# Kernel optimization log

Hardware: AMD Instinct MI355X
Metric: run time of the kernel (lower is better)

The kernel has to match this reference:

```python
import jax, jax.numpy as jnp
import numpy as np

N = 50000
E = 800000
IN_C, HID, LAT = 256, 128, 64


def setup_inputs() -> dict:
    key = jax.random.key(0)
    ks = jax.random.split(key, 8)
    x = jax.random.normal(ks[0], (N, IN_C), dtype=jnp.float32)
    edge_index = jax.random.randint(ks[1], (2, E), 0, N, dtype=jnp.int64)
    # Glorot-ish scaled weights (PyG GCNConv: Linear weight + separate bias)
    W1 = jax.random.normal(ks[2], (IN_C, HID), dtype=jnp.float32) / np.sqrt(IN_C)
    b1 = jnp.zeros((HID,), dtype=jnp.float32)
    Wmu = jax.random.normal(ks[3], (HID, LAT), dtype=jnp.float32) / np.sqrt(HID)
    bmu = jnp.zeros((LAT,), dtype=jnp.float32)
    Wlv = jax.random.normal(ks[4], (HID, LAT), dtype=jnp.float32) / np.sqrt(HID)
    blv = jnp.zeros((LAT,), dtype=jnp.float32)
    return {"x": x, "edge_index": edge_index, "W1": W1, "b1": b1,
            "Wmu": Wmu, "bmu": bmu, "Wlv": Wlv, "blv": blv}


def gcn_conv(x, edge_index, W, b):
    """PyG GCNConv: add self-loops, sym-normalize, transform, scatter-add."""
    n = x.shape[0]
    loop = jnp.arange(n, dtype=edge_index.dtype)
    row = jnp.concatenate([edge_index[0], loop])  # source
    col = jnp.concatenate([edge_index[1], loop])  # target
    deg = jax.ops.segment_sum(jnp.ones_like(col, dtype=x.dtype), col, num_segments=n)
    dinv = jax.lax.rsqrt(jnp.maximum(deg, 1e-12))  # deg >= 1 due to self-loops
    norm = dinv[row] * dinv[col]                   # [E+N]
    h = x @ W                                      # transform first (smaller width)
    msg = h[row] * norm[:, None]                   # [E+N, out] gathered messages
    out = jax.ops.segment_sum(msg, col, num_segments=n)
    return out + b


def reference(x, edge_index, W1, b1, Wmu, bmu, Wlv, blv):
    h = jax.nn.relu(gcn_conv(x, edge_index, W1, b1))
    # dropout p=0.0 -> identity
    mu = gcn_conv(h, edge_index, Wmu, bmu)
    logvar = gcn_conv(h, edge_index, Wlv, blv)
    return (mu, logvar)
```

## Files before the change

### kernel.cpp

```cpp
#include <hip/hip_runtime.h>
#include <stdint.h>

#define NN   50000
#define NE   800000
#define INC  256
#define HID  128
#define LAT  64

typedef unsigned short u16;
typedef short v8s __attribute__((ext_vector_type(8)));
typedef float v4f __attribute__((ext_vector_type(4)));

#define SLAB_OFF 0
#define OFFS_OFF 802816
#define W1P_OFF  881216
#define W2P_OFF  897600
#define G1_OFF   905792

#define NBIN        196
#define OFFS_STRIDE 200
#define NSLAB       784

#define G2_OFFU  8388608
#define C2_CNT   8388608
#define C2_DINV  8438608
#define C2_BKT   8488608

#define GB    782

__device__ __forceinline__ u16 f2b(float f) {
    union { float f; uint32_t i; } c; c.f = f;
    uint32_t r = c.i + 0x7FFF + ((c.i >> 16) & 1);
    return (u16)(r >> 16);
}
__device__ __forceinline__ float blo(unsigned u) { return __uint_as_float(u << 16); }
__device__ __forceinline__ float bhi(unsigned u) { return __uint_as_float(u & 0xffff0000u); }

__device__ void pack1_body(const float* __restrict__ W1, u16* __restrict__ W1P, int b) {
    int tg = b * 256 + threadIdx.x;
    int ks = tg >> 9, rem = tg & 511;
    int nt = rem >> 6, lane = rem & 63;
    int quad = lane >> 4, l15 = lane & 15;
    u16 o[8];
    #pragma unroll
    for (int j = 0; j < 8; j++)
        o[j] = f2b(W1[(long)(ks * 32 + quad * 8 + j) * HID + nt * 16 + l15]);
    *(ushort4*)(W1P + (long)tg * 8)     = make_ushort4(o[0], o[1], o[2], o[3]);
    *(ushort4*)(W1P + (long)tg * 8 + 4) = make_ushort4(o[4], o[5], o[6], o[7]);
}

__device__ void pack2_body(const float* __restrict__ Wmu, const float* __restrict__ Wlv,
                           u16* __restrict__ W2P, int b) {
    int tg = b * 256 + threadIdx.x;
    int ks = tg >> 9, rem = tg & 511;
    int nt = rem >> 6, lane = rem & 63;
    int quad = lane >> 4, l15 = lane & 15;
    const float* W = (nt < 4) ? Wmu : Wlv;
    int ntl = (nt < 4) ? nt : nt - 4;
    u16 o[8];
    #pragma unroll
    for (int j = 0; j < 8; j++)
        o[j] = f2b(W[(long)(ks * 32 + quad * 8 + j) * LAT + ntl * 16 + l15]);
    *(ushort4*)(W2P + (long)tg * 8)     = make_ushort4(o[0], o[1], o[2], o[3]);
    *(ushort4*)(W2P + (long)tg * 8 + 4) = make_ushort4(o[4], o[5], o[6], o[7]);
}

__global__ __launch_bounds__(256) void k_fusedA(unsigned* csr, const float* W1,
        const float* Wmu, const float* Wlv) {
    int b = blockIdx.x;
    if (b < 16) pack1_body(W1, (u16*)(csr + W1P_OFF), b);
    else pack2_body(Wmu, Wlv, (u16*)(csr + W2P_OFF), b - 16);
}

__device__ void gemm1_body(const float* __restrict__ xbuf,
        const unsigned* __restrict__ csr, u16* __restrict__ g1, int blk,
        u16* __restrict__ As) {
    const u16* W1P = (const u16*)(csr + W1P_OFF);
    int tid = threadIdx.x;
    int m0b = blk * 64;
    #pragma unroll
    for (int i = 0; i < 16; i++) {
        int idx = i * 256 + tid;
        int r = idx >> 6, c4 = idx & 63;
        int gr = m0b + r; gr = gr < NN ? gr : NN - 1;
        float4 a = *(const float4*)(xbuf + (long)gr * INC + c4 * 4);
        *(ushort4*)(As + r * 264 + c4 * 4) =
            make_ushort4(f2b(a.x), f2b(a.y), f2b(a.z), f2b(a.w));
    }
    __syncthreads();
    int lane = tid & 63, w = tid >> 6;
    int quad = lane >> 4, l15 = lane & 15;
    int m0 = m0b + w * 16;
    const v8s* bp = (const v8s*)W1P;
    v4f acc[8];
    #pragma unroll
    for (int t = 0; t < 8; t++) acc[t] = (v4f){0.f, 0.f, 0.f, 0.f};
    #pragma unroll
    for (int ks = 0; ks < 8; ks++) {
        v8s af = *(const v8s*)(As + (w * 16 + l15) * 264 + ks * 32 + quad * 8);
        #pragma unroll
        for (int t = 0; t < 8; t++) {
            v8s bf = bp[(ks * 8 + t) * 64 + lane];
            acc[t] = __builtin_amdgcn_mfma_f32_16x16x32_bf16(af, bf, acc[t], 0, 0, 0);
        }
    }
    #pragma unroll
    for (int r = 0; r < 4; r++) {
        int rr = m0 + quad * 4 + r;
        if (rr < NN) {
            u16* dst = g1 + (long)rr * HID + l15;
            #pragma unroll
            for (int t = 0; t < 8; t++) dst[t * 16] = f2b(acc[t][r]);
        }
    }
}

__device__ void part_body(const int* __restrict__ row, const int* __restrict__ col,
                          unsigned* __restrict__ csr, int id,
                          int* hist, int* scanbuf, unsigned* recs) {
    int tid = threadIdx.x;
    int base = id * 1024;
    hist[tid] = 0;
    __syncthreads();
    int v[4], u[4];
    #pragma unroll
    for (int i = 0; i < 4; i++) {
        int e = base + i * 256 + tid;
        if (e < NE) {
            v[i] = col[e]; u[i] = row[e];
            atomicAdd(&hist[v[i] >> 8], 1);
        } else v[i] = -1;
    }
    __syncthreads();
    int x = hist[tid];
    scanbuf[tid] = x;
    __syncthreads();
    for (int s = 1; s < 256; s <<= 1) {
        int y = (tid >= s) ? scanbuf[tid - s] : 0;
        __syncthreads();
        scanbuf[tid] += y;
        __syncthreads();
    }
    int excl = scanbuf[tid] - x;
    u16* offs = (u16*)(csr + OFFS_OFF) + (long)id * OFFS_STRIDE;
    if (tid <= NBIN) offs[tid] = (u16)excl;
    hist[tid] = excl;
    __syncthreads();
    #pragma unroll
    for (int i = 0; i < 4; i++) {
        if (v[i] >= 0) {
            int slot = atomicAdd(&hist[v[i] >> 8], 1);
            recs[slot] = (unsigned)u[i] | ((unsigned)(v[i] & 255) << 16);
        }
    }
    __syncthreads();
    unsigned* slab = csr + SLAB_OFF + (long)id * 1024;
    #pragma unroll
    for (int i = 0; i < 4; i++) slab[i * 256 + tid] = recs[i * 256 + tid];
}

__global__ __launch_bounds__(256) void k_fusedB(const float* __restrict__ xbuf,
        unsigned* __restrict__ csr, u16* __restrict__ g1,
        const int* __restrict__ row, const int* __restrict__ col) {
    __shared__ __align__(16) u16 As[64 * 264];
    __shared__ int hist[256];
    __shared__ int scanbuf[256];
    __shared__ unsigned recs[1024];
    int b = blockIdx.x;
    if (b < GB) gemm1_body(xbuf, csr, g1, b, As);
    part_body(row, col, csr, b, hist, scanbuf, recs);
}

__global__ __launch_bounds__(256) void k_merge(const unsigned* __restrict__ csr,
        unsigned* __restrict__ xb) {
    __shared__ int cnt_lds[256];
    __shared__ u16 bkt_lds[256 * 64];
    int tid = threadIdx.x;
    int bin = blockIdx.x;
    cnt_lds[tid] = 0;
    __syncthreads();
    const u16* offs = (const u16*)(csr + OFFS_OFF);
    const unsigned* slab = csr + SLAB_OFF;
    for (int s = tid; s < NSLAB; s += 256) {
        int st = offs[s * OFFS_STRIDE + bin];
        int en = offs[s * OFFS_STRIDE + bin + 1];
        for (int j = st; j < en; j++) {
            unsigned r = slab[s * 1024 + j];
            int vlo = (int)(r >> 16);
            int slot = atomicAdd(&cnt_lds[vlo], 1);
            if (slot < 64) bkt_lds[(vlo << 6) + slot] = (u16)(r & 0xffffu);
        }
    }
    __syncthreads();
    int* cnt2 = (int*)(xb + C2_CNT);
    float* dinv = (float*)(xb + C2_DINV);
    u16* bkt2 = (u16*)(xb + C2_BKT);
    int v0 = bin << 8;
    {
        int v = v0 + tid;
        if (v < NN) {
            int deg = cnt_lds[tid];
            int cn = deg < 64 ? deg : 64;
            cnt2[v] = cn;
            dinv[v] = rsqrtf((float)(deg + 1));
        }
    }
    const uint4* src = (const uint4*)bkt_lds;
    #pragma unroll
    for (int i = 0; i < 8; i++) {
        int idx = i * 256 + tid;
        int node = idx >> 3;
        if (v0 + node < NN)
            ((uint4*)(bkt2 + ((long)(v0 + node) << 6)))[idx & 7] = src[idx];
    }
}

#define ACC8(P, D, W) if (P) { \
    a0 += D * blo(W.x); a1 += D * bhi(W.x); a2 += D * blo(W.y); a3 += D * bhi(W.y); \
    a4 += D * blo(W.z); a5 += D * bhi(W.z); a6 += D * blo(W.w); a7 += D * bhi(W.w); }
#define RED(S) \
    a0 += __shfl_xor(a0, S); a1 += __shfl_xor(a1, S); a2 += __shfl_xor(a2, S); \
    a3 += __shfl_xor(a3, S); a4 += __shfl_xor(a4, S); a5 += __shfl_xor(a5, S); \
    a6 += __shfl_xor(a6, S); a7 += __shfl_xor(a7, S);
#define GATHER_LOOP(SRC) \
    for (int t = 0; t < cn; t += 32) { \
        int t0 = t + q, t1 = t0 + 4, t2 = t0 + 8,  t3 = t0 + 12, \
            t4 = t0 + 16, t5 = t0 + 20, t6 = t0 + 24, t7 = t0 + 28; \
        bool p0 = t0 < cn, p1 = t1 < cn, p2 = t2 < cn, p3 = t3 < cn, \
             p4 = t4 < cn, p5 = t5 < cn, p6 = t6 < cn, p7 = t7 < cn; \
        int u0 = __shfl(idx, t0), u1 = __shfl(idx, t1), u2 = __shfl(idx, t2), \
            u3 = __shfl(idx, t3), u4 = __shfl(idx, t4), u5 = __shfl(idx, t5), \
            u6 = __shfl(idx, t6), u7 = __shfl(idx, t7); \
        float d0 = __shfl(dvu, t0), d1 = __shfl(dvu, t1), d2 = __shfl(dvu, t2), \
              d3 = __shfl(dvu, t3), d4 = __shfl(dvu, t4), d5 = __shfl(dvu, t5), \
              d6 = __shfl(dvu, t6), d7 = __shfl(dvu, t7); \
        uint4 w0, w1, w2, w3, w4, w5, w6, w7; \
        if (p0) w0 = *(const uint4*)(SRC + (long)u0 * HID + c * 8); \
        if (p1) w1 = *(const uint4*)(SRC + (long)u1 * HID + c * 8); \
        if (p2) w2 = *(const uint4*)(SRC + (long)u2 * HID + c * 8); \
        if (p3) w3 = *(const uint4*)(SRC + (long)u3 * HID + c * 8); \
        if (p4) w4 = *(const uint4*)(SRC + (long)u4 * HID + c * 8); \
        if (p5) w5 = *(const uint4*)(SRC + (long)u5 * HID + c * 8); \
        if (p6) w6 = *(const uint4*)(SRC + (long)u6 * HID + c * 8); \
        if (p7) w7 = *(const uint4*)(SRC + (long)u7 * HID + c * 8); \
        ACC8(p0, d0, w0) \
        ACC8(p1, d1, w1) \
        ACC8(p2, d2, w2) \
        ACC8(p3, d3, w3) \
        ACC8(p4, d4, w4) \
        ACC8(p5, d5, w5) \
        ACC8(p6, d6, w6) \
        ACC8(p7, d7, w7) \
    }

#define HPAD 136
__global__ __launch_bounds__(256) void k_fusedD(const u16* __restrict__ g1,
        const unsigned* __restrict__ xb, const float* __restrict__ b1,
        const unsigned* __restrict__ csr, u16* __restrict__ g2) {
    __shared__ __align__(16) u16 hs[64 * HPAD];
    int tid = threadIdx.x;
    int lane = tid & 63, w = tid >> 6;
    int q = lane >> 4, c = lane & 15;
    const int* cnt2 = (const int*)(xb + C2_CNT);
    const float* dinv = (const float*)(xb + C2_DINV);
    const u16* bkt2 = (const u16*)(xb + C2_BKT);
    int m0b = blockIdx.x * 64;

    #pragma unroll 1
    for (int n = 0; n < 16; n++) {
        int v = m0b + w * 16 + n;
        int vc = v < NN ? v : NN - 1;
        int cn = cnt2[vc];
        float dvv = dinv[vc];
        int idx = (lane < cn) ? (int)bkt2[((long)vc << 6) + lane] : 0;
        float dvu = dinv[idx];
        float a0 = 0.f, a1 = 0.f, a2 = 0.f, a3 = 0.f,
              a4 = 0.f, a5 = 0.f, a6 = 0.f, a7 = 0.f;
        if (q == 0) {
            uint4 wv = *(const uint4*)(g1 + (long)vc * HID + c * 8);
            a0 = dvv * blo(wv.x); a1 = dvv * bhi(wv.x);
            a2 = dvv * blo(wv.y); a3 = dvv * bhi(wv.y);
            a4 = dvv * blo(wv.z); a5 = dvv * bhi(wv.z);
            a6 = dvv * blo(wv.w); a7 = dvv * bhi(wv.w);
        }
        GATHER_LOOP(g1)
        RED(16)
        RED(32)
        if (q == 0) {
            int j = c * 8;
            float r[8] = {a0, a1, a2, a3, a4, a5, a6, a7};
            unsigned p[4];
            #pragma unroll
            for (int i = 0; i < 4; i++) {
                float x0 = dvv * r[2 * i]     + b1[j + 2 * i];
                float x1 = dvv * r[2 * i + 1] + b1[j + 2 * i + 1];
                x0 = x0 > 0.f ? x0 : 0.f;
                x1 = x1 > 0.f ? x1 : 0.f;
                p[i] = (unsigned)f2b(x0) | ((unsigned)f2b(x1) << 16);
            }
            *(ushort4*)(hs + (w * 16 + n) * HPAD + j) =
                make_ushort4((u16)p[0], (u16)(p[0] >> 16), (u16)p[1], (u16)(p[1] >> 16));
            *(ushort4*)(hs + (w * 16 + n) * HPAD + j + 4) =
                make_ushort4((u16)p[2], (u16)(p[2] >> 16), (u16)p[3], (u16)(p[3] >> 16));
        }
    }
    __syncthreads();

    const u16* W2P = (const u16*)(csr + W2P_OFF);
    int quad = lane >> 4, l15 = lane & 15;
    int m0 = m0b + w * 16;
    const v8s* bp = (const v8s*)W2P;
    v4f acc[8];
    #pragma unroll
    for (int t = 0; t < 8; t++) acc[t] = (v4f){0.f, 0.f, 0.f, 0.f};
    #pragma unroll
    for (int ks = 0; ks < 4; ks++) {
        v8s af = *(const v8s*)(hs + (w * 16 + l15) * HPAD + ks * 32 + quad * 8);
        #pragma unroll
        for (int t = 0; t < 8; t++) {
            v8s bf = bp[(ks * 8 + t) * 64 + lane];
            acc[t] = __builtin_amdgcn_mfma_f32_16x16x32_bf16(af, bf, acc[t], 0, 0, 0);
        }
    }
    #pragma unroll
    for (int r = 0; r < 4; r++) {
        int rr = m0 + quad * 4 + r;
        if (rr < NN) {
            u16* dst = g2 + (long)rr * HID + l15;
            #pragma unroll
            for (int t = 0; t < 8; t++) dst[t * 16] = f2b(acc[t][r]);
        }
    }
}

__global__ __launch_bounds__(256) void k_gather2(const u16* __restrict__ g2,
        const unsigned* __restrict__ xb, const float* __restrict__ bmu,
        const float* __restrict__ blv, float* __restrict__ out) {
    int tid = threadIdx.x;
    int lane = tid & 63, w = tid >> 6;
    int v = blockIdx.x * 4 + w;
    int q = lane >> 4, c = lane & 15;
    const int* cnt2 = (const int*)(xb + C2_CNT);
    const float* dinv = (const float*)(xb + C2_DINV);
    const u16* bkt2 = (const u16*)(xb + C2_BKT);
    int cn = cnt2[v];
    float dvv = dinv[v];
    int idx = (lane < cn) ? (int)bkt2[((long)v << 6) + lane] : 0;
    float dvu = dinv[idx];
    float a0 = 0.f, a1 = 0.f, a2 = 0.f, a3 = 0.f, a4 = 0.f, a5 = 0.f, a6 = 0.f, a7 = 0.f;
    if (q == 0) {
        uint4 wv = *(const uint4*)(g2 + (long)v * HID + c * 8);
        a0 = dvv * blo(wv.x); a1 = dvv * bhi(wv.x); a2 = dvv * blo(wv.y); a3 = dvv * bhi(wv.y);
        a4 = dvv * blo(wv.z); a5 = dvv * bhi(wv.z); a6 = dvv * blo(wv.w); a7 = dvv * bhi(wv.w);
    }
    GATHER_LOOP(g2)
    RED(16)
    RED(32)
    if (q == 0) {
        float r[8] = {a0, a1, a2, a3, a4, a5, a6, a7};
        if (c < 8) {
            int j = c * 8;
            float4 o0 = make_float4(dvv * r[0] + bmu[j],     dvv * r[1] + bmu[j + 1],
                                    dvv * r[2] + bmu[j + 2], dvv * r[3] + bmu[j + 3]);
            float4 o1 = make_float4(dvv * r[4] + bmu[j + 4], dvv * r[5] + bmu[j + 5],
                                    dvv * r[6] + bmu[j + 6], dvv * r[7] + bmu[j + 7]);
            float* dst = out + (long)v * LAT + j;
            *(float4*)dst = o0;
            *(float4*)(dst + 4) = o1;
        } else {
            int j = c * 8 - 64;
            float4 o0 = make_float4(dvv * r[0] + blv[j],     dvv * r[1] + blv[j + 1],
                                    dvv * r[2] + blv[j + 2], dvv * r[3] + blv[j + 3]);
            float4 o1 = make_float4(dvv * r[4] + blv[j + 4], dvv * r[5] + blv[j + 5],
                                    dvv * r[6] + blv[j + 6], dvv * r[7] + blv[j + 7]);
            float* dst = out + (long)NN * LAT + (long)v * LAT + j;
            *(float4*)dst = o0;
            *(float4*)(dst + 4) = o1;
        }
    }
}

extern "C" void kernel_launch(void* const* d_in, const int* in_sizes, int n_in,
                              void* d_out, int out_size, void* d_ws, size_t ws_size,
                              hipStream_t stream) {
    float* xbuf = (float*)d_in[0];
    const int* ei  = (const int*)d_in[1];
    const float* W1  = (const float*)d_in[2];
    const float* b1  = (const float*)d_in[3];
    const float* Wmu = (const float*)d_in[4];
    const float* bmu = (const float*)d_in[5];
    const float* Wlv = (const float*)d_in[6];
    const float* blv = (const float*)d_in[7];
    const int* row = ei;
    const int* col = ei + NE;

    unsigned* csr = (unsigned*)d_out;
    u16* g1   = (u16*)(csr + G1_OFF);
    u16* g2   = (u16*)xbuf + G2_OFFU;
    unsigned* xb = (unsigned*)xbuf;

    k_fusedA<<<24, 256, 0, stream>>>(csr, W1, Wmu, Wlv);

    k_fusedB<<<NSLAB, 256, 0, stream>>>(xbuf, csr, g1, row, col);
    k_merge <<<NBIN, 256, 0, stream>>>(csr, xb);

    k_fusedD<<<GB, 256, 0, stream>>>(g1, xb, b1, csr, g2);

    k_gather2<<<NN / 4, 256, 0, stream>>>(g2, xb, bmu, blv, (float*)d_out);
}
```

Measured before the change: 220.3 us.

## Assign one 16-lane group per node in gather kernels, dropping shuffle reductions

Both gather stages switch from a full wavefront per node, with neighbour indices broadcast by shuffles and a cross-quarter shuffle reduction, to a 16-lane group per node that walks its neighbour list serially, four edges at a time. Each lane reads indices and dinv directly from memory. k_fusedD moves to 512 threads so 32 nodes are gathered per pass, and only the first 256 threads do the MFMA stage. k_gather2 handles 16 nodes per block. This removes the shuffle and reduction overhead and the lanes idled by predication, but it serializes each node's edge loop, adds redundant index loads, and leaves half the threads idle during the matmul phase.

```diff
diff --git a/kernel.cpp b/kernel.cpp
--- a/kernel.cpp
+++ b/kernel.cpp
@@ -215,120 +215,94 @@
     }
 }
 
-#define ACC8(P, D, W) if (P) { \
+#define EACC(D, W) { \
     a0 += D * blo(W.x); a1 += D * bhi(W.x); a2 += D * blo(W.y); a3 += D * bhi(W.y); \
     a4 += D * blo(W.z); a5 += D * bhi(W.z); a6 += D * blo(W.w); a7 += D * bhi(W.w); }
-#define RED(S) \
-    a0 += __shfl_xor(a0, S); a1 += __shfl_xor(a1, S); a2 += __shfl_xor(a2, S); \
-    a3 += __shfl_xor(a3, S); a4 += __shfl_xor(a4, S); a5 += __shfl_xor(a5, S); \
-    a6 += __shfl_xor(a6, S); a7 += __shfl_xor(a7, S);
-#define GATHER_LOOP(SRC) \
-    for (int t = 0; t < cn; t += 32) { \
-        int t0 = t + q, t1 = t0 + 4, t2 = t0 + 8,  t3 = t0 + 12, \
-            t4 = t0 + 16, t5 = t0 + 20, t6 = t0 + 24, t7 = t0 + 28; \
-        bool p0 = t0 < cn, p1 = t1 < cn, p2 = t2 < cn, p3 = t3 < cn, \
-             p4 = t4 < cn, p5 = t5 < cn, p6 = t6 < cn, p7 = t7 < cn; \
-        int u0 = __shfl(idx, t0), u1 = __shfl(idx, t1), u2 = __shfl(idx, t2), \
-            u3 = __shfl(idx, t3), u4 = __shfl(idx, t4), u5 = __shfl(idx, t5), \
-            u6 = __shfl(idx, t6), u7 = __shfl(idx, t7); \
-        float d0 = __shfl(dvu, t0), d1 = __shfl(dvu, t1), d2 = __shfl(dvu, t2), \
-              d3 = __shfl(dvu, t3), d4 = __shfl(dvu, t4), d5 = __shfl(dvu, t5), \
-              d6 = __shfl(dvu, t6), d7 = __shfl(dvu, t7); \
-        uint4 w0, w1, w2, w3, w4, w5, w6, w7; \
-        if (p0) w0 = *(const uint4*)(SRC + (long)u0 * HID + c * 8); \
-        if (p1) w1 = *(const uint4*)(SRC + (long)u1 * HID + c * 8); \
-        if (p2) w2 = *(const uint4*)(SRC + (long)u2 * HID + c * 8); \
-        if (p3) w3 = *(const uint4*)(SRC + (long)u3 * HID + c * 8); \
-        if (p4) w4 = *(const uint4*)(SRC + (long)u4 * HID + c * 8); \
-        if (p5) w5 = *(const uint4*)(SRC + (long)u5 * HID + c * 8); \
-        if (p6) w6 = *(const uint4*)(SRC + (long)u6 * HID + c * 8); \
-        if (p7) w7 = *(const uint4*)(SRC + (long)u7 * HID + c * 8); \
-        ACC8(p0, d0, w0) \
-        ACC8(p1, d1, w1) \
-        ACC8(p2, d2, w2) \
-        ACC8(p3, d3, w3) \
-        ACC8(p4, d4, w4) \
-        ACC8(p5, d5, w5) \
-        ACC8(p6, d6, w6) \
-        ACC8(p7, d7, w7) \
-    }
+
+#define GATHER_NODE(SRC) \
+    float a0, a1, a2, a3, a4, a5, a6, a7; \
+    { uint4 wv = *(const uint4*)(SRC + (long)vc * HID + lane16 * 8); \
+      a0 = dvv * blo(wv.x); a1 = dvv * bhi(wv.x); a2 = dvv * blo(wv.y); a3 = dvv * bhi(wv.y); \
+      a4 = dvv * blo(wv.z); a5 = dvv * bhi(wv.z); a6 = dvv * blo(wv.w); a7 = dvv * bhi(wv.w); } \
+    { const u16* bk = bkt2 + ((long)vc << 6); \
+      int e = 0; \
+      for (; e + 3 < cn; e += 4) { \
+          ushort4 ii = *(const ushort4*)(bk + e); \
+          float d0 = dinv[ii.x], d1 = dinv[ii.y], d2 = dinv[ii.z], d3 = dinv[ii.w]; \
+          uint4 w0 = *(const uint4*)(SRC + (long)ii.x * HID + lane16 * 8); \
+          uint4 w1 = *(const uint4*)(SRC + (long)ii.y * HID + lane16 * 8); \
+          uint4 w2 = *(const uint4*)(SRC + (long)ii.z * HID + lane16 * 8); \
+          uint4 w3 = *(const uint4*)(SRC + (long)ii.w * HID + lane16 * 8); \
+          EACC(d0, w0) EACC(d1, w1) EACC(d2, w2) EACC(d3, w3) \
+      } \
+      for (; e < cn; e++) { \
+          int i0 = bk[e]; \
+          float d0 = dinv[i0]; \
+          uint4 w0 = *(const uint4*)(SRC + (long)i0 * HID + lane16 * 8); \
+          EACC(d0, w0) \
+      } }
 
 #define HPAD 136
-__global__ __launch_bounds__(256) void k_fusedD(const u16* __restrict__ g1,
+__global__ __launch_bounds__(512, 4) void k_fusedD(const u16* __restrict__ g1,
         const unsigned* __restrict__ xb, const float* __restrict__ b1,
         const unsigned* __restrict__ csr, u16* __restrict__ g2) {
     __shared__ __align__(16) u16 hs[64 * HPAD];
     int tid = threadIdx.x;
-    int lane = tid & 63, w = tid >> 6;
-    int q = lane >> 4, c = lane & 15;
+    int lane16 = tid & 15, grp = tid >> 4;
     const int* cnt2 = (const int*)(xb + C2_CNT);
     const float* dinv = (const float*)(xb + C2_DINV);
     const u16* bkt2 = (const u16*)(xb + C2_BKT);
     int m0b = blockIdx.x * 64;
 
     #pragma unroll 1
-    for (int n = 0; n < 16; n++) {
-        int v = m0b + w * 16 + n;
+    for (int pass = 0; pass < 2; pass++) {
+        int nl = pass * 32 + grp;
+        int v = m0b + nl;
         int vc = v < NN ? v : NN - 1;
         int cn = cnt2[vc];
         float dvv = dinv[vc];
-        int idx = (lane < cn) ? (int)bkt2[((long)vc << 6) + lane] : 0;
-        float dvu = dinv[idx];
-        float a0 = 0.f, a1 = 0.f, a2 = 0.f, a3 = 0.f,
-              a4 = 0.f, a5 = 0.f, a6 = 0.f, a7 = 0.f;
-        if (q == 0) {
-            uint4 wv = *(const uint4*)(g1 + (long)vc * HID + c * 8);
-            a0 = dvv * blo(wv.x); a1 = dvv * bhi(wv.x);
-            a2 = dvv * blo(wv.y); a3 = dvv * bhi(wv.y);
-            a4 = dvv * blo(wv.z); a5 = dvv * bhi(wv.z);
-            a6 = dvv * blo(wv.w); a7 = dvv * bhi(wv.w);
-        }
-        GATHER_LOOP(g1)
-        RED(16)
-        RED(32)
-        if (q == 0) {
-            int j = c * 8;
-            float r[8] = {a0, a1, a2, a3, a4, a5, a6, a7};
-            unsigned p[4];
+        GATHER_NODE(g1)
+        int j = lane16 * 8;
+        float r[8] = {a0, a1, a2, a3, a4, a5, a6, a7};
+        unsigned p[4];
+        #pragma unroll
+        for (int i = 0; i < 4; i++) {
+            float x0 = dvv * r[2 * i]     + b1[j + 2 * i];
+            float x1 = dvv * r[2 * i + 1] + b1[j + 2 * i + 1];
+            x0 = x0 > 0.f ? x0 : 0.f;
+            x1 = x1 > 0.f ? x1 : 0.f;
+            p[i] = (unsigned)f2b(x0) | ((unsigned)f2b(x1) << 16);
+        }
+        *(uint4*)(hs + nl * HPAD + j) = make_uint4(p[0], p[1], p[2], p[3]);
+    }
+    __syncthreads();
+
+    if (tid < 256) {
+        const u16* W2P = (const u16*)(csr + W2P_OFF);
+        int lane = tid & 63, w = tid >> 6;
+        int quad = lane >> 4, l15 = lane & 15;
+        int m0 = m0b + w * 16;
+        const v8s* bp = (const v8s*)W2P;
+        v4f acc[8];
+        #pragma unroll
+        for (int t = 0; t < 8; t++) acc[t] = (v4f){0.f, 0.f, 0.f, 0.f};
+        #pragma unroll
+        for (int ks = 0; ks < 4; ks++) {
+            v8s af = *(const v8s*)(hs + (w * 16 + l15) * HPAD + ks * 32 + quad * 8);
             #pragma unroll
-            for (int i = 0; i < 4; i++) {
-                float x0 = dvv * r[2 * i]     + b1[j + 2 * i];
-                float x1 = dvv * r[2 * i + 1] + b1[j + 2 * i + 1];
-                x0 = x0 > 0.f ? x0 : 0.f;
-                x1 = x1 > 0.f ? x1 : 0.f;
-                p[i] = (unsigned)f2b(x0) | ((unsigned)f2b(x1) << 16);
+            for (int t = 0; t < 8; t++) {
+                v8s bf = bp[(ks * 8 + t) * 64 + lane];
+                acc[t] = __builtin_amdgcn_mfma_f32_16x16x32_bf16(af, bf, acc[t], 0, 0, 0);
             }
-            *(ushort4*)(hs + (w * 16 + n) * HPAD + j) =
-                make_ushort4((u16)p[0], (u16)(p[0] >> 16), (u16)p[1], (u16)(p[1] >> 16));
-            *(ushort4*)(hs + (w * 16 + n) * HPAD + j + 4) =
-                make_ushort4((u16)p[2], (u16)(p[2] >> 16), (u16)p[3], (u16)(p[3] >> 16));
-        }
-    }
-    __syncthreads();
-
-    const u16* W2P = (const u16*)(csr + W2P_OFF);
-    int quad = lane >> 4, l15 = lane & 15;
-    int m0 = m0b + w * 16;
-    const v8s* bp = (const v8s*)W2P;
-    v4f acc[8];
-    #pragma unroll
-    for (int t = 0; t < 8; t++) acc[t] = (v4f){0.f, 0.f, 0.f, 0.f};
-    #pragma unroll
-    for (int ks = 0; ks < 4; ks++) {
-        v8s af = *(const v8s*)(hs + (w * 16 + l15) * HPAD + ks * 32 + quad * 8);
-        #pragma unroll
-        for (int t = 0; t < 8; t++) {
-            v8s bf = bp[(ks * 8 + t) * 64 + lane];
-            acc[t] = __builtin_amdgcn_mfma_f32_16x16x32_bf16(af, bf, acc[t], 0, 0, 0);
-        }
-    }
-    #pragma unroll
-    for (int r = 0; r < 4; r++) {
-        int rr = m0 + quad * 4 + r;
-        if (rr < NN) {
-            u16* dst = g2 + (long)rr * HID + l15;
-            #pragma unroll
-            for (int t = 0; t < 8; t++) dst[t * 16] = f2b(acc[t][r]);
+        }
+        #pragma unroll
+        for (int r = 0; r < 4; r++) {
+            int rr = m0 + quad * 4 + r;
+            if (rr < NN) {
+                u16* dst = g2 + (long)rr * HID + l15;
+                #pragma unroll
+                for (int t = 0; t < 8; t++) dst[t * 16] = f2b(acc[t][r]);
+            }
         }
     }
 }
@@ -337,46 +311,33 @@
         const unsigned* __restrict__ xb, const float* __restrict__ bmu,
         const float* __restrict__ blv, float* __restrict__ out) {
     int tid = threadIdx.x;
-    int lane = tid & 63, w = tid >> 6;
-    int v = blockIdx.x * 4 + w;
-    int q = lane >> 4, c = lane & 15;
+    int lane16 = tid & 15, grp = tid >> 4;
+    int vc = blockIdx.x * 16 + grp;
     const int* cnt2 = (const int*)(xb + C2_CNT);
     const float* dinv = (const float*)(xb + C2_DINV);
     const u16* bkt2 = (const u16*)(xb + C2_BKT);
-    int cn = cnt2[v];
-    float dvv = dinv[v];
-    int idx = (lane < cn) ? (int)bkt2[((long)v << 6) + lane] : 0;
-    float dvu = dinv[idx];
-    float a0 = 0.f, a1 = 0.f, a2 = 0.f, a3 = 0.f, a4 = 0.f, a5 = 0.f, a6 = 0.f, a7 = 0.f;
-    if (q == 0) {
-        uint4 wv = *(const uint4*)(g2 + (long)v * HID + c * 8);
-        a0 = dvv * blo(wv.x); a1 = dvv * bhi(wv.x); a2 = dvv * blo(wv.y); a3 = dvv * bhi(wv.y);
-        a4 = dvv * blo(wv.z); a5 = dvv * bhi(wv.z); a6 = dvv * blo(wv.w); a7 = dvv * bhi(wv.w);
-    }
-    GATHER_LOOP(g2)
-    RED(16)
-    RED(32)
-    if (q == 0) {
-        float r[8] = {a0, a1, a2, a3, a4, a5, a6, a7};
-        if (c < 8) {
-            int j = c * 8;
-            float4 o0 = make_float4(dvv * r[0] + bmu[j],     dvv * r[1] + bmu[j + 1],
-                                    dvv * r[2] + bmu[j + 2], dvv * r[3] + bmu[j + 3]);
-            float4 o1 = make_float4(dvv * r[4] + bmu[j + 4], dvv * r[5] + bmu[j + 5],
-                                    dvv * r[6] + bmu[j + 6], dvv * r[7] + bmu[j + 7]);
-            float* dst = out + (long)v * LAT + j;
-            *(float4*)dst = o0;
-            *(float4*)(dst + 4) = o1;
-        } else {
-            int j = c * 8 - 64;
-            float4 o0 = make_float4(dvv * r[0] + blv[j],     dvv * r[1] + blv[j + 1],
-                                    dvv * r[2] + blv[j + 2], dvv * r[3] + blv[j + 3]);
-            float4 o1 = make_float4(dvv * r[4] + blv[j + 4], dvv * r[5] + blv[j + 5],
-                                    dvv * r[6] + blv[j + 6], dvv * r[7] + blv[j + 7]);
-            float* dst = out + (long)NN * LAT + (long)v * LAT + j;
-            *(float4*)dst = o0;
-            *(float4*)(dst + 4) = o1;
-        }
+    int cn = cnt2[vc];
+    float dvv = dinv[vc];
+    GATHER_NODE(g2)
+    float r[8] = {a0, a1, a2, a3, a4, a5, a6, a7};
+    if (lane16 < 8) {
+        int j = lane16 * 8;
+        float4 o0 = make_float4(dvv * r[0] + bmu[j],     dvv * r[1] + bmu[j + 1],
+                                dvv * r[2] + bmu[j + 2], dvv * r[3] + bmu[j + 3]);
+        float4 o1 = make_float4(dvv * r[4] + bmu[j + 4], dvv * r[5] + bmu[j + 5],
+                                dvv * r[6] + bmu[j + 6], dvv * r[7] + bmu[j + 7]);
+        float* dst = out + (long)vc * LAT + j;
+        *(float4*)dst = o0;
+        *(float4*)(dst + 4) = o1;
+    } else {
+        int j = lane16 * 8 - 64;
+        float4 o0 = make_float4(dvv * r[0] + blv[j],     dvv * r[1] + blv[j + 1],
+                                dvv * r[2] + blv[j + 2], dvv * r[3] + blv[j + 3]);
+        float4 o1 = make_float4(dvv * r[4] + blv[j + 4], dvv * r[5] + blv[j + 5],
+                                dvv * r[6] + blv[j + 6], dvv * r[7] + blv[j + 7]);
+        float* dst = out + (long)NN * LAT + (long)vc * LAT + j;
+        *(float4*)dst = o0;
+        *(float4*)(dst + 4) = o1;
     }
 }
 
@@ -404,7 +365,7 @@
     k_fusedB<<<NSLAB, 256, 0, stream>>>(xbuf, csr, g1, row, col);
     k_merge <<<NBIN, 256, 0, stream>>>(csr, xb);
 
-    k_fusedD<<<GB, 256, 0, stream>>>(g1, xb, b1, csr, g2);
-
-    k_gather2<<<NN / 4, 256, 0, stream>>>(g2, xb, bmu, blv, (float*)d_out);
-}
+    k_fusedD<<<GB, 512, 0, stream>>>(g1, xb, b1, csr, g2);
+
+    k_gather2<<<NN / 16, 256, 0, stream>>>(g2, xb, bmu, blv, (float*)d_out);
+}
```

Measured after the change: 209.5 us. -4.9%, faster.
